# Kernel optimization log

Measured on AMD Instinct MI355X. Metric: run time of the kernel, lower is better.

Reference implementation:

```python
import jax, jax.numpy as jnp
import numpy as np

D_MODEL = 1024
N_HEADS = 16
N_EXPERTS = 8
TOP_K = 2
EXPERT_HIDDEN = D_MODEL * 4 // N_EXPERTS  # 512, per MoELayer default


def layer_norm(x, g, b, eps=1e-5):
    mu = jnp.mean(x, axis=-1, keepdims=True)
    var = jnp.var(x, axis=-1, keepdims=True)
    return (x - mu) * jax.lax.rsqrt(var + eps) * g + b


def setup_inputs() -> dict:
    key = jax.random.key(0)
    ks = jax.random.split(key, 12)
    s = 1.0 / np.sqrt(D_MODEL)
    return {
        "x": jax.random.normal(ks[0], (2, 2048, D_MODEL), dtype=jnp.float32),
        "Wq": jax.random.normal(ks[1], (D_MODEL, D_MODEL), dtype=jnp.float32) * s,
        "Wk": jax.random.normal(ks[2], (D_MODEL, D_MODEL), dtype=jnp.float32) * s,
        "Wv": jax.random.normal(ks[3], (D_MODEL, D_MODEL), dtype=jnp.float32) * s,
        "Wo": jax.random.normal(ks[4], (D_MODEL, D_MODEL), dtype=jnp.float32) * s,
        "g1": jnp.ones((D_MODEL,), jnp.float32),
        "b1": jnp.zeros((D_MODEL,), jnp.float32),
        "g2": jnp.ones((D_MODEL,), jnp.float32),
        "b2": jnp.zeros((D_MODEL,), jnp.float32),
        "Wg": jax.random.normal(ks[5], (D_MODEL, N_EXPERTS), dtype=jnp.float32) * s,
        "W1": jax.random.normal(ks[6], (N_EXPERTS, D_MODEL, EXPERT_HIDDEN), dtype=jnp.float32) * s,
        "W2": jax.random.normal(ks[7], (N_EXPERTS, EXPERT_HIDDEN, D_MODEL), dtype=jnp.float32) * (1.0 / np.sqrt(EXPERT_HIDDEN)),
    }


def reference(x, Wq, Wk, Wv, Wo, g1, b1, g2, b2, Wg, W1, W2):
    B, S, D = x.shape
    H, dk = N_HEADS, D // N_HEADS

    # ---- pre-norm attention + residual (dropout = identity in eval) ----
    xn = layer_norm(x, g1, b1)
    q = (xn @ Wq).reshape(B, S, H, dk).transpose(0, 2, 1, 3)  # [B,H,S,dk]
    k = (xn @ Wk).reshape(B, S, H, dk).transpose(0, 2, 1, 3)
    v = (xn @ Wv).reshape(B, S, H, dk).transpose(0, 2, 1, 3)
    scores = jnp.einsum("bhqd,bhkd->bhqk", q, k) / np.sqrt(dk)
    attn = jax.nn.softmax(scores, axis=-1)
    o = jnp.einsum("bhqk,bhkd->bhqd", attn, v)
    o = o.transpose(0, 2, 1, 3).reshape(B, S, D) @ Wo
    x = x + o

    # ---- pre-norm MoE + residual ----
    xn2 = layer_norm(x, g2, b2)
    xf = xn2.reshape(B * S, D)  # [T, D]
    gate = xf @ Wg  # [T, E]
    topv, topi = jax.lax.top_k(gate, TOP_K)  # [T, K]
    probs = jax.nn.softmax(topv, axis=-1)    # softmax over top-k scores
    # dense combine weights [T, E] (top-k indices are distinct)
    cw = jnp.sum(jax.nn.one_hot(topi, N_EXPERTS, dtype=xf.dtype) * probs[..., None], axis=1)
    h = jax.nn.relu(jnp.einsum("td,edh->teh", xf, W1))  # [T,E,Hid]
    y = jnp.einsum("teh,ehd->ted", h, W2)               # [T,E,D]
    moe = jnp.einsum("ted,te->td", y, cw).reshape(B, S, D)
    return x + moe
```

## Files before the change

### kernel.cpp

```cpp
#include <hip/hip_runtime.h>

typedef __attribute__((ext_vector_type(8))) _Float16 f16x8;
typedef __attribute__((ext_vector_type(4))) _Float16 f16x4;
typedef __attribute__((ext_vector_type(2))) _Float16 f16x2;
typedef __attribute__((ext_vector_type(2))) __fp16 fp16x2_n;
typedef __attribute__((ext_vector_type(8))) short bf16x8;
typedef __attribute__((ext_vector_type(4))) float f32x4;
typedef __attribute__((ext_vector_type(4))) unsigned short u16x4;
typedef __attribute__((ext_vector_type(4))) float fx4;

#define D_MODEL 1024
#define N_HEADS 16
#define SEQ 2048
#define TOKENS 4096
#define N_EXP 8
#define EHID 512
#define LO_S 2048.0f
#define INV_LO (1.0f / 2048.0f)
#define QSCALE 0.18033688011112043f
#define DTHR 11.0f

__device__ inline unsigned short f2bf(float f) {
  union { float f; unsigned u; } v; v.f = f;
  unsigned u = v.u;
  return (unsigned short)((u + 0x7FFFu + ((u >> 16) & 1u)) >> 16);
}

__device__ inline float bf2f(unsigned short b) {
  union { unsigned u; float f; } v; v.u = ((unsigned)b) << 16;
  return v.f;
}

__device__ inline void split16(float v, _Float16& h, _Float16& l) {
  h = (_Float16)v;
  l = (_Float16)((v - (float)h) * LO_S);
}

__device__ inline void split2(float a, float b, f16x2& h, f16x2& l) {
  fp16x2_n hn = __builtin_amdgcn_cvt_pkrtz(a, b);
  h = __builtin_bit_cast(f16x2, hn);
  fp16x2_n ln = __builtin_amdgcn_cvt_pkrtz((a - (float)h[0]) * LO_S, (b - (float)h[1]) * LO_S);
  l = __builtin_bit_cast(f16x2, ln);
}

__device__ inline void gload_lds16(const void* g, void* lds) {
  __builtin_amdgcn_global_load_lds((const __attribute__((address_space(1))) void*)g,
                                   (__attribute__((address_space(3))) void*)lds, 16, 0, 0);
}

__global__ __launch_bounds__(256) void prep_ln_kernel(const float* __restrict__ x, const float* __restrict__ g1,
                                                      const float* __restrict__ b1,
                                                      _Float16* __restrict__ xh, _Float16* __restrict__ xl,
                                                      const float* __restrict__ Wq, const float* __restrict__ Wk,
                                                      const float* __restrict__ Wv, const float* __restrict__ Wo,
                                                      const float* __restrict__ W1, const float* __restrict__ W2,
                                                      _Float16* __restrict__ qkvh, _Float16* __restrict__ qkvl,
                                                      _Float16* __restrict__ woh, _Float16* __restrict__ wol,
                                                      unsigned short* __restrict__ W1T, unsigned short* __restrict__ W2T,
                                                      int* __restrict__ cnt, int* __restrict__ perm) {
  int bb = blockIdx.x;
  if (bb < 4096) {
    int t = bb, tid = threadIdx.x;
    const float* row = x + (size_t)t * D_MODEL;
    fx4 v = *(const fx4*)(row + tid * 4);
    float s = v[0] + v[1] + v[2] + v[3];
    float s2 = v[0]*v[0] + v[1]*v[1] + v[2]*v[2] + v[3]*v[3];
    #pragma unroll
    for (int off = 1; off < 64; off <<= 1) { s += __shfl_xor(s, off); s2 += __shfl_xor(s2, off); }
    __shared__ float red[8];
    int wv = tid >> 6, wl = tid & 63;
    if (wl == 0) { red[wv] = s; red[4 + wv] = s2; }
    __syncthreads();
    s = red[0] + red[1] + red[2] + red[3];
    s2 = red[4] + red[5] + red[6] + red[7];
    float mu = s * (1.f / 1024.f);
    float var = s2 * (1.f / 1024.f) - mu * mu;
    float rstd = rsqrtf(var + 1e-5f);
    int kk = tid * 4;
    f16x4 oh, ol;
    #pragma unroll
    for (int c = 0; c < 4; c++) {
      float y = (v[c] - mu) * rstd * g1[kk + c] + b1[kk + c];
      _Float16 h, lo; split16(y, h, lo);
      oh[c] = h; ol[c] = lo;
    }
    *(f16x4*)(xh + (size_t)t * D_MODEL + kk) = oh;
    *(f16x4*)(xl + (size_t)t * D_MODEL + kk) = ol;
    return;
  }
  int b = bb - 4096;
  if (b >= 12288) {
    int i = (b - 12288) * 256 + threadIdx.x;
    if (i < 8) cnt[i] = 0;
    if (i < 8704) perm[i] = 0;
    return;
  }
  __shared__ float tile[32][33];
  int tx = threadIdx.x & 31, ty = threadIdx.x >> 5;
  if (b < 4096) {
    int z = b >> 10, rem = b & 1023;
    int c0 = (rem & 31) * 32, r0 = (rem >> 5) * 32;
    const float* src = (z == 0) ? Wq : (z == 1) ? Wk : (z == 2) ? Wv : Wo;
    _Float16* dh = (z < 3) ? qkvh + (size_t)z * 1048576 : woh;
    _Float16* dl = (z < 3) ? qkvl + (size_t)z * 1048576 : wol;
    #pragma unroll
    for (int i = 0; i < 4; i++) tile[ty + 8*i][tx] = src[(size_t)(r0 + ty + 8*i) * 1024 + c0 + tx];
    __syncthreads();
    #pragma unroll
    for (int i = 0; i < 4; i++) {
      float v = tile[tx][ty + 8*i];
      _Float16 h, lo; split16(v, h, lo);
      size_t idx = (size_t)(c0 + ty + 8*i) * 1024 + r0 + tx;
      dh[idx] = h; dl[idx] = lo;
    }
  } else if (b < 8192) {
    int q = b - 4096, z = q >> 9, rem = q & 511;
    int c0 = (rem & 15) * 32, r0 = (rem >> 4) * 32;
    const float* src = W1 + (size_t)z * 524288;
    unsigned short* dst = W1T + (size_t)z * 524288;
    #pragma unroll
    for (int i = 0; i < 4; i++) tile[ty + 8*i][tx] = src[(size_t)(r0 + ty + 8*i) * 512 + c0 + tx];
    __syncthreads();
    #pragma unroll
    for (int i = 0; i < 4; i++) dst[(size_t)(c0 + ty + 8*i) * 1024 + r0 + tx] = f2bf(tile[tx][ty + 8*i]);
  } else {
    int q = b - 8192, z = q >> 9, rem = q & 511;
    int c0 = (rem & 31) * 32, r0 = (rem >> 5) * 32;
    const float* src = W2 + (size_t)z * 524288;
    unsigned short* dst = W2T + (size_t)z * 524288;
    #pragma unroll
    for (int i = 0; i < 4; i++) tile[ty + 8*i][tx] = src[(size_t)(r0 + ty + 8*i) * 1024 + c0 + tx];
    __syncthreads();
    #pragma unroll
    for (int i = 0; i < 4; i++) dst[(size_t)(c0 + ty + 8*i) * 512 + r0 + tx] = f2bf(tile[tx][ty + 8*i]);
  }
}

__device__ inline void gemm128s(const _Float16* __restrict__ Ah, const _Float16* __restrict__ Al,
                                const _Float16* __restrict__ Bh, const _Float16* __restrict__ Bl,
                                int lda, int ldb, int K, int bm, int bn,
                                _Float16* lsbuf, f32x4 (&acc)[4][4], f32x4 (&accx)[4][4]) {
  const int tid = threadIdx.x, w = tid >> 6, l = tid & 63, lr = l & 15, lg = l >> 4;
  const int wr = (w >> 1) * 64, wc = (w & 1) * 64;
  int ca = (((tid & 3) ^ ((tid >> 3) & 3)) * 8);
  int ra0 = tid >> 2, ra1 = 64 + (tid >> 2);
  const _Float16* gA0 = Ah + (size_t)(bm + ra0) * lda + ca;
  const _Float16* gA1 = Ah + (size_t)(bm + ra1) * lda + ca;
  const _Float16* gA2 = Al + (size_t)(bm + ra0) * lda + ca;
  const _Float16* gA3 = Al + (size_t)(bm + ra1) * lda + ca;
  const _Float16* gB0 = Bh + (size_t)(bn + ra0) * ldb + ca;
  const _Float16* gB1 = Bh + (size_t)(bn + ra1) * ldb + ca;
  const _Float16* gB2 = Bl + (size_t)(bn + ra0) * ldb + ca;
  const _Float16* gB3 = Bl + (size_t)(bn + ra1) * ldb + ca;
  char* base = (char*)lsbuf;
  const int wo = w * 1024;
#define STAGE8(bb_, ko) do { \
    gload_lds16(gA0 + (ko), (bb_) + wo);         gload_lds16(gA1 + (ko), (bb_) + 4096 + wo);  \
    gload_lds16(gA2 + (ko), (bb_) + 8192 + wo);  gload_lds16(gA3 + (ko), (bb_) + 12288 + wo); \
    gload_lds16(gB0 + (ko), (bb_) + 16384 + wo); gload_lds16(gB1 + (ko), (bb_) + 20480 + wo); \
    gload_lds16(gB2 + (ko), (bb_) + 24576 + wo); gload_lds16(gB3 + (ko), (bb_) + 28672 + wo); } while (0)
  STAGE8(base, 0);
  __syncthreads();
  const int swzB = ((lg ^ ((lr >> 1) & 3)) << 4);
  int cur = 0;
  for (int ko = 0; ko < K; ko += 32) {
    char* bR = base + cur * 32768;
    if (ko + 32 < K) STAGE8(base + (cur ^ 1) * 32768, ko + 32);
    f16x8 ah[4], al4[4], bh4[4], bl4[4];
    #pragma unroll
    for (int m = 0; m < 4; m++) {
      int roff = (wr + m * 16 + lr) * 64 + swzB;
      ah[m]  = *(const f16x8*)(bR + roff);
      al4[m] = *(const f16x8*)(bR + 8192 + roff);
    }
    #pragma unroll
    for (int n = 0; n < 4; n++) {
      int roff = (wc + n * 16 + lr) * 64 + swzB;
      bh4[n] = *(const f16x8*)(bR + 16384 + roff);
      bl4[n] = *(const f16x8*)(bR + 24576 + roff);
    }
    __builtin_amdgcn_s_setprio(1);
    #pragma unroll
    for (int m = 0; m < 4; m++)
      #pragma unroll
      for (int n = 0; n < 4; n++) {
        acc[m][n]  = __builtin_amdgcn_mfma_f32_16x16x32_f16(ah[m], bh4[n], acc[m][n], 0, 0, 0);
        accx[m][n] = __builtin_amdgcn_mfma_f32_16x16x32_f16(ah[m], bl4[n], accx[m][n], 0, 0, 0);
        accx[m][n] = __builtin_amdgcn_mfma_f32_16x16x32_f16(al4[m], bh4[n], accx[m][n], 0, 0, 0);
      }
    __builtin_amdgcn_s_setprio(0);
    __syncthreads();
    cur ^= 1;
  }
#undef STAGE8
}

__global__ __launch_bounds__(256) void gemm_qkv_kernel(const _Float16* __restrict__ xh, const _Float16* __restrict__ xl,
                                                       const _Float16* __restrict__ Wh, const _Float16* __restrict__ Wl,
                                                       _Float16* __restrict__ qh, _Float16* __restrict__ ql,
                                                       _Float16* __restrict__ kh, _Float16* __restrict__ kl,
                                                       _Float16* __restrict__ vh, _Float16* __restrict__ vl) {
  __shared__ _Float16 ls[32768];
  f32x4 acc[4][4] = {}, accx[4][4] = {};
  int bid = blockIdx.x;
  int sw = (bid & 7) * 96 + (bid >> 3);
  int bm = (sw & 31) * 128, bn = (sw >> 5) * 128;
  gemm128s(xh, xl, Wh, Wl, 1024, 1024, 1024, bm, bn, ls, acc, accx);
  const int tid = threadIdx.x, w = tid >> 6, l = tid & 63, lr = l & 15, lg = l >> 4;
  const int wr = (w >> 1) * 64, wc = (w & 1) * 64;
  #pragma unroll
  for (int m = 0; m < 4; m++) {
    int row0 = bm + wr + m * 16 + lg * 4;
    #pragma unroll
    for (int n = 0; n < 4; n++) {
      int col = bn + wc + n * 16 + lr;
      int mat = col >> 10;
      int c = col & 1023, h = c >> 6, d = c & 63;
      if (mat == 2) {
        int bb = row0 >> 11, ss = row0 & 2047;
        int tile = ss >> 5, kvs = ss & 31;
        f16x4 ph, pl;
        #pragma unroll
        for (int j = 0; j < 4; j++) {
          float v = acc[m][n][j] + accx[m][n][j] * INV_LO;
          _Float16 hh, ll; split16(v, hh, ll);
          ph[j] = hh; pl[j] = ll;
        }
        size_t base = ((size_t)(bb * N_HEADS + h) * 64 + tile) * 2048;
        int off = d * 32 + ((((kvs >> 3) ^ ((d >> 1) & 3)) << 3) | (kvs & 7));
        *(f16x4*)(vh + base + off) = ph;
        *(f16x4*)(vl + base + off) = pl;
      } else if (mat == 1) {
        #pragma unroll
        for (int j = 0; j < 4; j++) {
          float v = acc[m][n][j] + accx[m][n][j] * INV_LO;
          _Float16 hh, ll; split16(v, hh, ll);
          int t = row0 + j, bb = t >> 11, ss = t & 2047;
          int tile = ss >> 5, r = ss & 31;
          size_t base = ((size_t)(bb * N_HEADS + h) * 64 + tile) * 2048;
          int off = r * 64 + ((((d >> 3) ^ (r & 7)) << 3) | (d & 7));
          kh[base + off] = hh; kl[base + off] = ll;
        }
      } else {
        #pragma unroll
        for (int j = 0; j < 4; j++) {
          float v = (acc[m][n][j] + accx[m][n][j] * INV_LO) * QSCALE;
          _Float16 hh, ll; split16(v, hh, ll);
          int t = row0 + j, bb = t >> 11, ss = t & 2047;
          size_t idx = ((size_t)(bb * N_HEADS + h) * SEQ + ss) * 64 + d;
          qh[idx] = hh; ql[idx] = ll;
        }
      }
    }
  }
}

__global__ __launch_bounds__(256, 4) void flash_kernel(const _Float16* __restrict__ qhp, const _Float16* __restrict__ qlp,
                                                       const _Float16* __restrict__ khs, const _Float16* __restrict__ kls,
                                                       const _Float16* __restrict__ vhs, const _Float16* __restrict__ vls,
                                                       _Float16* __restrict__ oh, _Float16* __restrict__ ol) {
  __shared__ _Float16 lsKV[2][8192];
  __shared__ _Float16 lsP[4][2][512];
  int wgid = blockIdx.x;
  int xcd = wgid & 7, kk = wgid >> 3;
  int bh = xcd * 4 + (kk >> 5), qt = kk & 31;
  int tid = threadIdx.x, w = tid >> 6, l = tid & 63, lr = l & 15, lg = l >> 4;
  int q0 = qt * 64 + w * 16;
  const _Float16* qhb = qhp + (size_t)bh * SEQ * 64;
  const _Float16* qlb = qlp + (size_t)bh * SEQ * 64;
  f16x8 qfh[2], qfl[2];
  #pragma unroll
  for (int ks = 0; ks < 2; ks++) {
    size_t idx = (size_t)(q0 + lr) * 64 + ks * 32 + lg * 8;
    qfh[ks] = *(const f16x8*)(qhb + idx);
    qfl[ks] = *(const f16x8*)(qlb + idx);
  }
  const _Float16* splane = (w == 0) ? khs : (w == 1) ? kls : (w == 2) ? vhs : vls;
  const _Float16* sbase = splane + (size_t)bh * 131072 + l * 8;

  f32x4 acc[4] = {}, accx[4] = {};
  float mst = -1e30f, lstp = 0.f;

  {
    const _Float16* sp = sbase;
    _Float16* dd = &lsKV[0][w * 2048];
    gload_lds16(sp, dd); gload_lds16(sp + 512, dd + 512);
    gload_lds16(sp + 1024, dd + 1024); gload_lds16(sp + 1536, dd + 1536);
  }
  __syncthreads();

  for (int t = 0; t < 64; t++) {
    int bR = t & 1;
    if (t < 63) {
      const _Float16* sp = sbase + (size_t)(t + 1) * 2048;
      _Float16* dd = &lsKV[bR ^ 1][w * 2048];
      gload_lds16(sp, dd); gload_lds16(sp + 512, dd + 512);
      gload_lds16(sp + 1024, dd + 1024); gload_lds16(sp + 1536, dd + 1536);
    }
    char* bufB = (char*)&lsKV[bR][0];

    f32x4 s[2] = {}, sx[2] = {};
    #pragma unroll
    for (int ks = 0; ks < 2; ks++) {
      f16x8 kfh[2], kfl[2];
      #pragma unroll
      for (int m = 0; m < 2; m++) {
        int off = (m * 16 + lr) * 128 + (((ks * 4 + lg) ^ (lr & 7)) << 4);
        kfh[m] = *(const f16x8*)(bufB + off);
        kfl[m] = *(const f16x8*)(bufB + 4096 + off);
      }
      __builtin_amdgcn_s_setprio(1);
      #pragma unroll
      for (int m = 0; m < 2; m++) {
        s[m]  = __builtin_amdgcn_mfma_f32_16x16x32_f16(kfh[m], qfh[ks], s[m], 0, 0, 0);
        sx[m] = __builtin_amdgcn_mfma_f32_16x16x32_f16(kfh[m], qfl[ks], sx[m], 0, 0, 0);
        sx[m] = __builtin_amdgcn_mfma_f32_16x16x32_f16(kfl[m], qfh[ks], sx[m], 0, 0, 0);
      }
      __builtin_amdgcn_s_setprio(0);
    }

    float tm = -3e38f;
    #pragma unroll
    for (int m = 0; m < 2; m++)
      #pragma unroll
      for (int j = 0; j < 4; j++) {
        s[m][j] += sx[m][j] * INV_LO;
        tm = fmaxf(tm, s[m][j]);
      }
    if (!__all(tm - mst <= DTHR)) {
      tm = fmaxf(tm, __shfl_xor(tm, 16));
      tm = fmaxf(tm, __shfl_xor(tm, 32));
      float mnew = fmaxf(mst, tm);
      float corr = exp2f(mst - mnew);
      #pragma unroll
      for (int m2 = 0; m2 < 4; m2++)
        #pragma unroll
        for (int j = 0; j < 4; j++) { acc[m2][j] *= corr; accx[m2][j] *= corr; }
      lstp *= corr;
      mst = mnew;
    }
    #pragma unroll
    for (int m = 0; m < 2; m++) {
      #pragma unroll
      for (int j = 0; j < 4; j++) {
        float p = exp2f(s[m][j] - mst);
        lstp += p;
        s[m][j] = p;
      }
      f16x2 h01, h23, l01, l23;
      split2(s[m][0], s[m][1], h01, l01);
      split2(s[m][2], s[m][3], h23, l23);
      f16x4 ph, pl;
      ph[0] = h01[0]; ph[1] = h01[1]; ph[2] = h23[0]; ph[3] = h23[1];
      pl[0] = l01[0]; pl[1] = l01[1]; pl[2] = l23[0]; pl[3] = l23[1];
      int boff = lr * 64 + ((((m * 2 + (lg >> 1)) ^ ((lr >> 1) & 3)) << 4) | ((lg & 1) * 8));
      *(f16x4*)((char*)&lsP[w][0][0] + boff) = ph;
      *(f16x4*)((char*)&lsP[w][1][0] + boff) = pl;
    }

    int poff = lr * 64 + ((lg ^ ((lr >> 1) & 3)) << 4);
    f16x8 pfh = *(const f16x8*)((char*)&lsP[w][0][0] + poff);
    f16x8 pfl = *(const f16x8*)((char*)&lsP[w][1][0] + poff);
    __builtin_amdgcn_s_setprio(1);
    #pragma unroll
    for (int m2 = 0; m2 < 4; m2++) {
      int voff = (m2 * 16 + lr) * 64 + ((lg ^ ((lr >> 1) & 3)) << 4);
      f16x8 vfh = *(const f16x8*)(bufB + 8192 + voff);
      f16x8 vfl = *(const f16x8*)(bufB + 12288 + voff);
      acc[m2]  = __builtin_amdgcn_mfma_f32_16x16x32_f16(vfh, pfh, acc[m2], 0, 0, 0);
      accx[m2] = __builtin_amdgcn_mfma_f32_16x16x32_f16(vfh, pfl, accx[m2], 0, 0, 0);
      accx[m2] = __builtin_amdgcn_mfma_f32_16x16x32_f16(vfl, pfh, accx[m2], 0, 0, 0);
    }
    __builtin_amdgcn_s_setprio(0);
    __syncthreads();
  }

  float lst = lstp + __shfl_xor(lstp, 16);
  lst += __shfl_xor(lst, 32);
  float inv = 1.f / lst;
  int b = bh >> 4, h = bh & 15;
  int tkn = b * SEQ + q0 + lr;
  #pragma unroll
  for (int m2 = 0; m2 < 4; m2++) {
    f16x4 ph, pl;
    #pragma unroll
    for (int j = 0; j < 4; j++) {
      float o = (acc[m2][j] + accx[m2][j] * INV_LO) * inv;
      _Float16 hh, ll; split16(o, hh, ll);
      ph[j] = hh; pl[j] = ll;
    }
    size_t idx = (size_t)tkn * D_MODEL + h * 64 + m2 * 16 + lg * 4;
    *(f16x4*)(oh + idx) = ph;
    *(f16x4*)(ol + idx) = pl;
  }
}

__global__ __launch_bounds__(256) void gemm_oproj_kernel(const _Float16* __restrict__ ah, const _Float16* __restrict__ al,
                                                         const _Float16* __restrict__ Wh, const _Float16* __restrict__ Wl,
                                                         const float* __restrict__ x, float* __restrict__ out) {
  __shared__ _Float16 ls[32768];
  f32x4 acc[4][4] = {}, accx[4][4] = {};
  int bid = blockIdx.x;
  int sw = (bid & 7) * 32 + (bid >> 3);
  int bm = (sw & 31) * 128, bn = (sw >> 5) * 128;
  gemm128s(ah, al, Wh, Wl, 1024, 1024, 1024, bm, bn, ls, acc, accx);
  const int tid = threadIdx.x, w = tid >> 6, l = tid & 63, lr = l & 15, lg = l >> 4;
  const int wr = (w >> 1) * 64, wc = (w & 1) * 64;
  #pragma unroll
  for (int m = 0; m < 4; m++) {
    int row0 = bm + wr + m * 16 + lg * 4;
    #pragma unroll
    for (int n = 0; n < 4; n++) {
      int col = bn + wc + n * 16 + lr;
      #pragma unroll
      for (int j = 0; j < 4; j++) {
        size_t idx = (size_t)(row0 + j) * D_MODEL + col;
        out[idx] = (acc[m][n][j] + accx[m][n][j] * INV_LO) + x[idx];
      }
    }
  }
}

__global__ __launch_bounds__(256) void gate_kernel(const float* __restrict__ x1, const float* __restrict__ Wg,
                                                   const float* __restrict__ g2, const float* __restrict__ b2,
                                                   unsigned short* __restrict__ xn2,
                                                   int* __restrict__ cnt, int* __restrict__ topi,
                                                   float* __restrict__ topw) {
  int t = blockIdx.x * 4 + (threadIdx.x >> 6);
  int l = threadIdx.x & 63;
  const float* row = x1 + (size_t)t * D_MODEL;
  fx4 v[4];
  float s = 0.f, s2 = 0.f;
  #pragma unroll
  for (int i = 0; i < 4; i++) {
    v[i] = *(const fx4*)(row + l * 16 + i * 4);
    #pragma unroll
    for (int c = 0; c < 4; c++) { s += v[i][c]; s2 += v[i][c] * v[i][c]; }
  }
  #pragma unroll
  for (int off = 1; off < 64; off <<= 1) { s += __shfl_xor(s, off); s2 += __shfl_xor(s2, off); }
  float mu = s * (1.f / 1024.f);
  float var = s2 * (1.f / 1024.f) - mu * mu;
  float rstd = rsqrtf(var + 1e-5f);
  float a8[8] = {0,0,0,0,0,0,0,0};
  #pragma unroll
  for (int i = 0; i < 4; i++) {
    u16x4 ox;
    #pragma unroll
    for (int c = 0; c < 4; c++) {
      int kk = l * 16 + i * 4 + c;
      float xv = (v[i][c] - mu) * rstd * g2[kk] + b2[kk];
      ox[c] = f2bf(xv);
      const float* wr_ = Wg + (size_t)kk * 8;
      fx4 wa = *(const fx4*)wr_;
      fx4 wb = *(const fx4*)(wr_ + 4);
      a8[0] += xv * wa[0]; a8[1] += xv * wa[1]; a8[2] += xv * wa[2]; a8[3] += xv * wa[3];
      a8[4] += xv * wb[0]; a8[5] += xv * wb[1]; a8[6] += xv * wb[2]; a8[7] += xv * wb[3];
    }
    *(u16x4*)(xn2 + (size_t)t * D_MODEL + l * 16 + i * 4) = ox;
  }
  #pragma unroll
  for (int e = 0; e < 8; e++)
    #pragma unroll
    for (int off = 1; off < 64; off <<= 1) a8[e] += __shfl_xor(a8[e], off);
  if (l == 0) {
    int i0 = 0; float v0 = a8[0];
    #pragma unroll
    for (int e = 1; e < 8; e++) if (a8[e] > v0) { v0 = a8[e]; i0 = e; }
    int i1 = -1; float v1 = -3.4e38f;
    #pragma unroll
    for (int e = 0; e < 8; e++) if (e != i0 && a8[e] > v1) { v1 = a8[e]; i1 = e; }
    float p0 = 1.f / (1.f + __expf(v1 - v0));
    topi[t * 2] = i0; topi[t * 2 + 1] = i1;
    topw[t * 2] = p0; topw[t * 2 + 1] = 1.f - p0;
    atomicAdd(&cnt[i0], 1); atomicAdd(&cnt[i1], 1);
  }
}

__global__ __launch_bounds__(256) void scatter_kernel(const int* __restrict__ topi, const int* __restrict__ cnt,
                                                      int* __restrict__ perm, int* __restrict__ slot_of) {
  int e = blockIdx.x, tid = threadIdx.x;
  __shared__ int basesh;
  __shared__ int wsum[4];
  if (tid == 0) {
    int a = 0;
    for (int i = 0; i < e; i++) a += ((cnt[i] + 63) >> 6) << 6;
    basesh = a;
  }
  __syncthreads();
  for (int seg = 0; seg < 8192; seg += 256) {
    int a = seg + tid;
    int match = (topi[a] == e) ? 1 : 0;
    unsigned long long bal = __ballot(match);
    int wl = tid & 63, wv = tid >> 6;
    int lanepre = __popcll(bal & ((1ULL << wl) - 1ULL));
    if (wl == 0) wsum[wv] = __popcll(bal);
    __syncthreads();
    int wpre = 0;
    for (int i = 0; i < wv; i++) wpre += wsum[i];
    int total = wsum[0] + wsum[1] + wsum[2] + wsum[3];
    if (match) {
      int pos = basesh + wpre + lanepre;
      perm[pos] = a >> 1;
      slot_of[a] = pos;
    }
    __syncthreads();
    if (tid == 0) basesh += total;
    __syncthreads();
  }
}

__global__ __launch_bounds__(512) void moe_ffn_kernel(const unsigned short* __restrict__ xn2,
                                                      const unsigned short* __restrict__ W1T,
                                                      const unsigned short* __restrict__ W2T,
                                                      const int* __restrict__ cnt,
                                                      const int* __restrict__ perm,
                                                      unsigned short* __restrict__ y) {
  int bid = blockIdx.x;
  int e = -1, lt = bid, off = 0;
  for (int i = 0; i < 8; i++) {
    int nt = (cnt[i] + 63) >> 6;
    if (lt < nt) { e = i; break; }
    lt -= nt; off += nt << 6;
  }
  if (e < 0) return;
  int slot0 = off + lt * 64;

  __shared__ int t_sh[64];
  __shared__ unsigned short lsX[64 * 128];
  __shared__ unsigned short hsh[64 * 264];
  int tid = threadIdx.x, w = tid >> 6, l = tid & 63, lr = l & 15, lg = l >> 4;
  if (tid < 64) t_sh[tid] = perm[slot0 + tid];
  __syncthreads();

  const unsigned short* W1e = W1T + (size_t)e * EHID * D_MODEL;
  const unsigned short* W2e = W2T + (size_t)e * D_MODEL * EHID;

  f32x4 acc2[4][8] = {};
  for (int h = 0; h < 2; h++) {
    f32x4 acc1[4][2] = {};
    for (int kc = 0; kc < 8; kc++) {
      __syncthreads();
      #pragma unroll
      for (int L = 0; L < 2; L++) {
        int u = tid + 512 * L;
        int r = u >> 4, sp = u & 15;
        int cs = (sp & 8) | ((sp & 7) ^ (r & 7));
        gload_lds16(xn2 + (size_t)t_sh[r] * D_MODEL + kc * 128 + cs * 8, (char*)lsX + u * 16);
      }
      __syncthreads();
      #pragma unroll
      for (int kst = 0; kst < 4; kst++) {
        bf16x8 a[4];
        #pragma unroll
        for (int m = 0; m < 4; m++) {
          int row = m * 16 + lr;
          int slot = kst * 4 + lg;
          int cs = (slot & 8) | ((slot & 7) ^ (row & 7));
          a[m] = *(const bf16x8*)((char*)lsX + row * 256 + cs * 16);
        }
        int ko = kc * 128 + kst * 32;
        #pragma unroll
        for (int n = 0; n < 2; n++) {
          bf16x8 bb = *(const bf16x8*)(W1e + (size_t)(h * 256 + w * 32 + n * 16 + lr) * D_MODEL + ko + lg * 8);
          #pragma unroll
          for (int m = 0; m < 4; m++)
            acc1[m][n] = __builtin_amdgcn_mfma_f32_16x16x32_bf16(a[m], bb, acc1[m][n], 0, 0, 0);
        }
      }
    }
    __syncthreads();
    #pragma unroll
    for (int m = 0; m < 4; m++)
      #pragma unroll
      for (int n = 0; n < 2; n++)
        #pragma unroll
        for (int j = 0; j < 4; j++)
          hsh[(m*16 + lg*4 + j) * 264 + w * 32 + n * 16 + lr] = f2bf(fmaxf(acc1[m][n][j], 0.f));
    __syncthreads();
    for (int k2 = 0; k2 < 256; k2 += 32) {
      bf16x8 a2[4];
      #pragma unroll
      for (int m = 0; m < 4; m++) a2[m] = *(const bf16x8*)(hsh + (m*16 + lr) * 264 + k2 + lg * 8);
      #pragma unroll
      for (int n = 0; n < 8; n++) {
        bf16x8 bb = *(const bf16x8*)(W2e + (size_t)(w * 128 + n * 16 + lr) * EHID + h * 256 + k2 + lg * 8);
        #pragma unroll
        for (int m = 0; m < 4; m++)
          acc2[m][n] = __builtin_amdgcn_mfma_f32_16x16x32_bf16(a2[m], bb, acc2[m][n], 0, 0, 0);
      }
    }
  }
  #pragma unroll
  for (int m = 0; m < 4; m++)
    #pragma unroll
    for (int j = 0; j < 4; j++) {
      int r = m * 16 + lg * 4 + j;
      #pragma unroll
      for (int n = 0; n < 8; n++)
        y[(size_t)(slot0 + r) * D_MODEL + w * 128 + n * 16 + lr] = f2bf(acc2[m][n][j]);
    }
}

__global__ __launch_bounds__(256) void combine_kernel(const unsigned short* __restrict__ y, const int* __restrict__ slot_of,
                                                      const float* __restrict__ topw, float* __restrict__ out) {
  int t = blockIdx.x * 4 + (threadIdx.x >> 6);
  int l = threadIdx.x & 63;
  int s0 = slot_of[t * 2], s1 = slot_of[t * 2 + 1];
  float w0 = topw[t * 2], w1 = topw[t * 2 + 1];
  const unsigned short* y0 = y + (size_t)s0 * D_MODEL + l * 16;
  const unsigned short* y1 = y + (size_t)s1 * D_MODEL + l * 16;
  float* o = out + (size_t)t * D_MODEL + l * 16;
  #pragma unroll
  for (int i = 0; i < 4; i++) {
    u16x4 av = *(const u16x4*)(y0 + i * 4);
    u16x4 bv = *(const u16x4*)(y1 + i * 4);
    fx4 d = *(const fx4*)(o + i * 4);
    #pragma unroll
    for (int j = 0; j < 4; j++) d[j] += w0 * bf2f(av[j]) + w1 * bf2f(bv[j]);
    *(fx4*)(o + i * 4) = d;
  }
}

#define MB (1u << 20)
extern "C" void kernel_launch(void* const* d_in, const int* in_sizes, int n_in,
                              void* d_out, int out_size, void* d_ws, size_t ws_size,
                              hipStream_t stream) {
  const float* x  = (const float*)d_in[0];
  const float* Wq = (const float*)d_in[1];
  const float* Wk = (const float*)d_in[2];
  const float* Wv = (const float*)d_in[3];
  const float* Wo = (const float*)d_in[4];
  const float* g1 = (const float*)d_in[5];
  const float* b1 = (const float*)d_in[6];
  const float* g2 = (const float*)d_in[7];
  const float* b2 = (const float*)d_in[8];
  const float* Wg = (const float*)d_in[9];
  const float* W1 = (const float*)d_in[10];
  const float* W2 = (const float*)d_in[11];
  float* out = (float*)d_out;

  char* ws = (char*)d_ws;
  _Float16* xn1h = (_Float16*)(ws + 0*MB);
  _Float16* xn1l = (_Float16*)(ws + 8*MB);
  _Float16* Wqkh = (_Float16*)(ws + 16*MB);
  _Float16* Wqkl = (_Float16*)(ws + 22*MB);
  _Float16* Woh  = (_Float16*)(ws + 28*MB);
  _Float16* Wol  = (_Float16*)(ws + 30*MB);
  _Float16* qhb  = (_Float16*)(ws + 32*MB);
  _Float16* qlb  = (_Float16*)(ws + 40*MB);
  _Float16* khb  = (_Float16*)(ws + 48*MB);
  _Float16* klb  = (_Float16*)(ws + 56*MB);
  _Float16* vhb  = (_Float16*)(ws + 64*MB);
  _Float16* vlb  = (_Float16*)(ws + 72*MB);
  unsigned short* xn2 = (unsigned short*)(ws + 80*MB);
  unsigned short* W1T = (unsigned short*)(ws + 88*MB);
  unsigned short* W2T = (unsigned short*)(ws + 96*MB);
  char* misc = ws + 104*MB;
  int*   topi    = (int*)(misc);
  float* topw    = (float*)(misc + 32768);
  int*   slot_of = (int*)(misc + 65536);
  int*   cnt     = (int*)(misc + 98304);
  int*   perm    = (int*)(misc + 98368);
  unsigned short* ybuf = (unsigned short*)(ws + 32*MB);
  _Float16* attnh = xn1h;
  _Float16* attnl = xn1l;

  prep_ln_kernel<<<16419, 256, 0, stream>>>(x, g1, b1, xn1h, xn1l,
                                            Wq, Wk, Wv, Wo, W1, W2,
                                            Wqkh, Wqkl, Woh, Wol, W1T, W2T, cnt, perm);

  gemm_qkv_kernel<<<768, 256, 0, stream>>>(xn1h, xn1l, Wqkh, Wqkl, qhb, qlb, khb, klb, vhb, vlb);
  flash_kernel<<<1024, 256, 0, stream>>>(qhb, qlb, khb, klb, vhb, vlb, attnh, attnl);
  gemm_oproj_kernel<<<256, 256, 0, stream>>>(attnh, attnl, Woh, Wol, x, out);

  gate_kernel<<<1024, 256, 0, stream>>>(out, Wg, g2, b2, xn2, cnt, topi, topw);
  scatter_kernel<<<8, 256, 0, stream>>>(topi, cnt, perm, slot_of);
  moe_ffn_kernel<<<136, 512, 0, stream>>>(xn2, W1T, W2T, cnt, perm, ybuf);
  combine_kernel<<<1024, 256, 0, stream>>>(ybuf, slot_of, topw, out);

  (void)in_sizes; (void)n_in; (void)out_size; (void)ws_size;
}
```

Measured before the change: 526.5 us.

## Process two query tiles per flash block and parallelize MoE scatter by segment

The flash attention kernel now handles 128 query rows per workgroup (two 64-row sub-tiles) instead of 64. Each K/V tile loaded into LDS is therefore reused twice, which halves global K/V traffic and the grid size. The MoE scatter is split into 64 blocks (expert × segment) using per-segment counts gathered in the gate kernel, replacing 8 serial blocks. The costs are higher register pressure in flash, fewer workgroups to fill the GPU, and extra atomics in the gate kernel.

Result: slower. 647.4 us (+23.0%).

```diff
diff --git a/kernel.cpp b/kernel.cpp
--- a/kernel.cpp
+++ b/kernel.cpp
@@ -57,7 +57,8 @@
                                                       _Float16* __restrict__ qkvh, _Float16* __restrict__ qkvl,
                                                       _Float16* __restrict__ woh, _Float16* __restrict__ wol,
                                                       unsigned short* __restrict__ W1T, unsigned short* __restrict__ W2T,
-                                                      int* __restrict__ cnt, int* __restrict__ perm) {
+                                                      int* __restrict__ cnt, int* __restrict__ cnt8,
+                                                      int* __restrict__ perm) {
   int bb = blockIdx.x;
   if (bb < 4096) {
     int t = bb, tid = threadIdx.x;
@@ -92,6 +93,7 @@
   if (b >= 12288) {
     int i = (b - 12288) * 256 + threadIdx.x;
     if (i < 8) cnt[i] = 0;
+    if (i < 64) cnt8[i] = 0;
     if (i < 8704) perm[i] = 0;
     return;
   }
@@ -263,23 +265,25 @@
   __shared__ _Float16 lsP[4][2][512];
   int wgid = blockIdx.x;
   int xcd = wgid & 7, kk = wgid >> 3;
-  int bh = xcd * 4 + (kk >> 5), qt = kk & 31;
+  int bh = xcd * 4 + (kk >> 4), qt = kk & 15;
   int tid = threadIdx.x, w = tid >> 6, l = tid & 63, lr = l & 15, lg = l >> 4;
-  int q0 = qt * 64 + w * 16;
+  int q0 = qt * 128 + w * 16;
   const _Float16* qhb = qhp + (size_t)bh * SEQ * 64;
   const _Float16* qlb = qlp + (size_t)bh * SEQ * 64;
-  f16x8 qfh[2], qfl[2];
-  #pragma unroll
-  for (int ks = 0; ks < 2; ks++) {
-    size_t idx = (size_t)(q0 + lr) * 64 + ks * 32 + lg * 8;
-    qfh[ks] = *(const f16x8*)(qhb + idx);
-    qfl[ks] = *(const f16x8*)(qlb + idx);
-  }
+  f16x8 qfh[2][2], qfl[2][2];
+  #pragma unroll
+  for (int tq = 0; tq < 2; tq++)
+    #pragma unroll
+    for (int ks = 0; ks < 2; ks++) {
+      size_t idx = (size_t)(q0 + tq * 64 + lr) * 64 + ks * 32 + lg * 8;
+      qfh[tq][ks] = *(const f16x8*)(qhb + idx);
+      qfl[tq][ks] = *(const f16x8*)(qlb + idx);
+    }
   const _Float16* splane = (w == 0) ? khs : (w == 1) ? kls : (w == 2) ? vhs : vls;
   const _Float16* sbase = splane + (size_t)bh * 131072 + l * 8;
 
-  f32x4 acc[4] = {}, accx[4] = {};
-  float mst = -1e30f, lstp = 0.f;
+  f32x4 acc[2][4] = {}, accx[2][4] = {};
+  float mst[2] = {-1e30f, -1e30f}, lstp[2] = {0.f, 0.f};
 
   {
     const _Float16* sp = sbase;
@@ -299,99 +303,105 @@
     }
     char* bufB = (char*)&lsKV[bR][0];
 
-    f32x4 s[2] = {}, sx[2] = {};
-    #pragma unroll
-    for (int ks = 0; ks < 2; ks++) {
-      f16x8 kfh[2], kfl[2];
+    #pragma unroll
+    for (int tq = 0; tq < 2; tq++) {
+      f32x4 s[2] = {}, sx[2] = {};
+      #pragma unroll
+      for (int ks = 0; ks < 2; ks++) {
+        f16x8 kfh[2], kfl[2];
+        #pragma unroll
+        for (int m = 0; m < 2; m++) {
+          int off = (m * 16 + lr) * 128 + (((ks * 4 + lg) ^ (lr & 7)) << 4);
+          kfh[m] = *(const f16x8*)(bufB + off);
+          kfl[m] = *(const f16x8*)(bufB + 4096 + off);
+        }
+        __builtin_amdgcn_s_setprio(1);
+        #pragma unroll
+        for (int m = 0; m < 2; m++) {
+          s[m]  = __builtin_amdgcn_mfma_f32_16x16x32_f16(kfh[m], qfh[tq][ks], s[m], 0, 0, 0);
+          sx[m] = __builtin_amdgcn_mfma_f32_16x16x32_f16(kfh[m], qfl[tq][ks], sx[m], 0, 0, 0);
+          sx[m] = __builtin_amdgcn_mfma_f32_16x16x32_f16(kfl[m], qfh[tq][ks], sx[m], 0, 0, 0);
+        }
+        __builtin_amdgcn_s_setprio(0);
+      }
+
+      float tm = -3e38f;
+      #pragma unroll
+      for (int m = 0; m < 2; m++)
+        #pragma unroll
+        for (int j = 0; j < 4; j++) {
+          s[m][j] += sx[m][j] * INV_LO;
+          tm = fmaxf(tm, s[m][j]);
+        }
+      if (!__all(tm - mst[tq] <= DTHR)) {
+        tm = fmaxf(tm, __shfl_xor(tm, 16));
+        tm = fmaxf(tm, __shfl_xor(tm, 32));
+        float mnew = fmaxf(mst[tq], tm);
+        float corr = exp2f(mst[tq] - mnew);
+        #pragma unroll
+        for (int m2 = 0; m2 < 4; m2++)
+          #pragma unroll
+          for (int j = 0; j < 4; j++) { acc[tq][m2][j] *= corr; accx[tq][m2][j] *= corr; }
+        lstp[tq] *= corr;
+        mst[tq] = mnew;
+      }
       #pragma unroll
       for (int m = 0; m < 2; m++) {
-        int off = (m * 16 + lr) * 128 + (((ks * 4 + lg) ^ (lr & 7)) << 4);
-        kfh[m] = *(const f16x8*)(bufB + off);
-        kfl[m] = *(const f16x8*)(bufB + 4096 + off);
-      }
+        #pragma unroll
+        for (int j = 0; j < 4; j++) {
+          float p = exp2f(s[m][j] - mst[tq]);
+          lstp[tq] += p;
+          s[m][j] = p;
+        }
+        f16x2 h01, h23, l01, l23;
+        split2(s[m][0], s[m][1], h01, l01);
+        split2(s[m][2], s[m][3], h23, l23);
+        f16x4 ph, pl;
+        ph[0] = h01[0]; ph[1] = h01[1]; ph[2] = h23[0]; ph[3] = h23[1];
+        pl[0] = l01[0]; pl[1] = l01[1]; pl[2] = l23[0]; pl[3] = l23[1];
+        int boff = lr * 64 + ((((m * 2 + (lg >> 1)) ^ ((lr >> 1) & 3)) << 4) | ((lg & 1) * 8));
+        *(f16x4*)((char*)&lsP[w][0][0] + boff) = ph;
+        *(f16x4*)((char*)&lsP[w][1][0] + boff) = pl;
+      }
+
+      int poff = lr * 64 + ((lg ^ ((lr >> 1) & 3)) << 4);
+      f16x8 pfh = *(const f16x8*)((char*)&lsP[w][0][0] + poff);
+      f16x8 pfl = *(const f16x8*)((char*)&lsP[w][1][0] + poff);
       __builtin_amdgcn_s_setprio(1);
       #pragma unroll
-      for (int m = 0; m < 2; m++) {
-        s[m]  = __builtin_amdgcn_mfma_f32_16x16x32_f16(kfh[m], qfh[ks], s[m], 0, 0, 0);
-        sx[m] = __builtin_amdgcn_mfma_f32_16x16x32_f16(kfh[m], qfl[ks], sx[m], 0, 0, 0);
-        sx[m] = __builtin_amdgcn_mfma_f32_16x16x32_f16(kfl[m], qfh[ks], sx[m], 0, 0, 0);
+      for (int m2 = 0; m2 < 4; m2++) {
+        int voff = (m2 * 16 + lr) * 64 + ((lg ^ ((lr >> 1) & 3)) << 4);
+        f16x8 vfh = *(const f16x8*)(bufB + 8192 + voff);
+        f16x8 vfl = *(const f16x8*)(bufB + 12288 + voff);
+        acc[tq][m2]  = __builtin_amdgcn_mfma_f32_16x16x32_f16(vfh, pfh, acc[tq][m2], 0, 0, 0);
+        accx[tq][m2] = __builtin_amdgcn_mfma_f32_16x16x32_f16(vfh, pfl, accx[tq][m2], 0, 0, 0);
+        accx[tq][m2] = __builtin_amdgcn_mfma_f32_16x16x32_f16(vfl, pfh, accx[tq][m2], 0, 0, 0);
       }
       __builtin_amdgcn_s_setprio(0);
     }
-
-    float tm = -3e38f;
-    #pragma unroll
-    for (int m = 0; m < 2; m++)
+    __syncthreads();
+  }
+
+  int b = bh >> 4, h = bh & 15;
+  #pragma unroll
+  for (int tq = 0; tq < 2; tq++) {
+    float lst = lstp[tq] + __shfl_xor(lstp[tq], 16);
+    lst += __shfl_xor(lst, 32);
+    float inv = 1.f / lst;
+    int tkn = b * SEQ + q0 + tq * 64 + lr;
+    #pragma unroll
+    for (int m2 = 0; m2 < 4; m2++) {
+      f16x4 ph, pl;
       #pragma unroll
       for (int j = 0; j < 4; j++) {
-        s[m][j] += sx[m][j] * INV_LO;
-        tm = fmaxf(tm, s[m][j]);
-      }
-    if (!__all(tm - mst <= DTHR)) {
-      tm = fmaxf(tm, __shfl_xor(tm, 16));
-      tm = fmaxf(tm, __shfl_xor(tm, 32));
-      float mnew = fmaxf(mst, tm);
-      float corr = exp2f(mst - mnew);
-      #pragma unroll
-      for (int m2 = 0; m2 < 4; m2++)
-        #pragma unroll
-        for (int j = 0; j < 4; j++) { acc[m2][j] *= corr; accx[m2][j] *= corr; }
-      lstp *= corr;
-      mst = mnew;
-    }
-    #pragma unroll
-    for (int m = 0; m < 2; m++) {
-      #pragma unroll
-      for (int j = 0; j < 4; j++) {
-        float p = exp2f(s[m][j] - mst);
-        lstp += p;
-        s[m][j] = p;
-      }
-      f16x2 h01, h23, l01, l23;
-      split2(s[m][0], s[m][1], h01, l01);
-      split2(s[m][2], s[m][3], h23, l23);
-      f16x4 ph, pl;
-      ph[0] = h01[0]; ph[1] = h01[1]; ph[2] = h23[0]; ph[3] = h23[1];
-      pl[0] = l01[0]; pl[1] = l01[1]; pl[2] = l23[0]; pl[3] = l23[1];
-      int boff = lr * 64 + ((((m * 2 + (lg >> 1)) ^ ((lr >> 1) & 3)) << 4) | ((lg & 1) * 8));
-      *(f16x4*)((char*)&lsP[w][0][0] + boff) = ph;
-      *(f16x4*)((char*)&lsP[w][1][0] + boff) = pl;
-    }
-
-    int poff = lr * 64 + ((lg ^ ((lr >> 1) & 3)) << 4);
-    f16x8 pfh = *(const f16x8*)((char*)&lsP[w][0][0] + poff);
-    f16x8 pfl = *(const f16x8*)((char*)&lsP[w][1][0] + poff);
-    __builtin_amdgcn_s_setprio(1);
-    #pragma unroll
-    for (int m2 = 0; m2 < 4; m2++) {
-      int voff = (m2 * 16 + lr) * 64 + ((lg ^ ((lr >> 1) & 3)) << 4);
-      f16x8 vfh = *(const f16x8*)(bufB + 8192 + voff);
-      f16x8 vfl = *(const f16x8*)(bufB + 12288 + voff);
-      acc[m2]  = __builtin_amdgcn_mfma_f32_16x16x32_f16(vfh, pfh, acc[m2], 0, 0, 0);
-      accx[m2] = __builtin_amdgcn_mfma_f32_16x16x32_f16(vfh, pfl, accx[m2], 0, 0, 0);
-      accx[m2] = __builtin_amdgcn_mfma_f32_16x16x32_f16(vfl, pfh, accx[m2], 0, 0, 0);
-    }
-    __builtin_amdgcn_s_setprio(0);
-    __syncthreads();
-  }
-
-  float lst = lstp + __shfl_xor(lstp, 16);
-  lst += __shfl_xor(lst, 32);
-  float inv = 1.f / lst;
-  int b = bh >> 4, h = bh & 15;
-  int tkn = b * SEQ + q0 + lr;
-  #pragma unroll
-  for (int m2 = 0; m2 < 4; m2++) {
-    f16x4 ph, pl;
-    #pragma unroll
-    for (int j = 0; j < 4; j++) {
-      float o = (acc[m2][j] + accx[m2][j] * INV_LO) * inv;
-      _Float16 hh, ll; split16(o, hh, ll);
-      ph[j] = hh; pl[j] = ll;
-    }
-    size_t idx = (size_t)tkn * D_MODEL + h * 64 + m2 * 16 + lg * 4;
-    *(f16x4*)(oh + idx) = ph;
-    *(f16x4*)(ol + idx) = pl;
+        float o = (acc[tq][m2][j] + accx[tq][m2][j] * INV_LO) * inv;
+        _Float16 hh, ll; split16(o, hh, ll);
+        ph[j] = hh; pl[j] = ll;
+      }
+      size_t idx = (size_t)tkn * D_MODEL + h * 64 + m2 * 16 + lg * 4;
+      *(f16x4*)(oh + idx) = ph;
+      *(f16x4*)(ol + idx) = pl;
+    }
   }
 }
 
@@ -424,8 +434,8 @@
 __global__ __launch_bounds__(256) void gate_kernel(const float* __restrict__ x1, const float* __restrict__ Wg,
                                                    const float* __restrict__ g2, const float* __restrict__ b2,
                                                    unsigned short* __restrict__ xn2,
-                                                   int* __restrict__ cnt, int* __restrict__ topi,
-                                                   float* __restrict__ topw) {
+                                                   int* __restrict__ cnt, int* __restrict__ cnt8,
+                                                   int* __restrict__ topi, float* __restrict__ topw) {
   int t = blockIdx.x * 4 + (threadIdx.x >> 6);
   int l = threadIdx.x & 63;
   const float* row = x1 + (size_t)t * D_MODEL;
@@ -473,23 +483,29 @@
     float p0 = 1.f / (1.f + __expf(v1 - v0));
     topi[t * 2] = i0; topi[t * 2 + 1] = i1;
     topw[t * 2] = p0; topw[t * 2 + 1] = 1.f - p0;
+    int seg = t >> 9;
     atomicAdd(&cnt[i0], 1); atomicAdd(&cnt[i1], 1);
+    atomicAdd(&cnt8[i0 * 8 + seg], 1); atomicAdd(&cnt8[i1 * 8 + seg], 1);
   }
 }
 
 __global__ __launch_bounds__(256) void scatter_kernel(const int* __restrict__ topi, const int* __restrict__ cnt,
+                                                      const int* __restrict__ cnt8,
                                                       int* __restrict__ perm, int* __restrict__ slot_of) {
-  int e = blockIdx.x, tid = threadIdx.x;
+  int e = blockIdx.x & 7, seg = blockIdx.x >> 3;
+  int tid = threadIdx.x;
   __shared__ int basesh;
   __shared__ int wsum[4];
   if (tid == 0) {
     int a = 0;
     for (int i = 0; i < e; i++) a += ((cnt[i] + 63) >> 6) << 6;
+    for (int s = 0; s < seg; s++) a += cnt8[e * 8 + s];
     basesh = a;
   }
   __syncthreads();
-  for (int seg = 0; seg < 8192; seg += 256) {
-    int a = seg + tid;
+  int a0 = seg * 1024;
+  for (int segi = 0; segi < 1024; segi += 256) {
+    int a = a0 + segi + tid;
     int match = (topi[a] == e) ? 1 : 0;
     unsigned long long bal = __ballot(match);
     int wl = tid & 63, wv = tid >> 6;
@@ -661,21 +677,22 @@
   float* topw    = (float*)(misc + 32768);
   int*   slot_of = (int*)(misc + 65536);
   int*   cnt     = (int*)(misc + 98304);
-  int*   perm    = (int*)(misc + 98368);
+  int*   cnt8    = (int*)(misc + 98368);
+  int*   perm    = (int*)(misc + 98688);
   unsigned short* ybuf = (unsigned short*)(ws + 32*MB);
   _Float16* attnh = xn1h;
   _Float16* attnl = xn1l;
 
   prep_ln_kernel<<<16419, 256, 0, stream>>>(x, g1, b1, xn1h, xn1l,
                                             Wq, Wk, Wv, Wo, W1, W2,
-                                            Wqkh, Wqkl, Woh, Wol, W1T, W2T, cnt, perm);
+                                            Wqkh, Wqkl, Woh, Wol, W1T, W2T, cnt, cnt8, perm);
 
   gemm_qkv_kernel<<<768, 256, 0, stream>>>(xn1h, xn1l, Wqkh, Wqkl, qhb, qlb, khb, klb, vhb, vlb);
-  flash_kernel<<<1024, 256, 0, stream>>>(qhb, qlb, khb, klb, vhb, vlb, attnh, attnl);
+  flash_kernel<<<512, 256, 0, stream>>>(qhb, qlb, khb, klb, vhb, vlb, attnh, attnl);
   gemm_oproj_kernel<<<256, 256, 0, stream>>>(attnh, attnl, Woh, Wol, x, out);
 
-  gate_kernel<<<1024, 256, 0, stream>>>(out, Wg, g2, b2, xn2, cnt, topi, topw);
-  scatter_kernel<<<8, 256, 0, stream>>>(topi, cnt, perm, slot_of);
+  gate_kernel<<<1024, 256, 0, stream>>>(out, Wg, g2, b2, xn2, cnt, cnt8, topi, topw);
+  scatter_kernel<<<64, 256, 0, stream>>>(topi, cnt, cnt8, perm, slot_of);
   moe_ffn_kernel<<<136, 512, 0, stream>>>(xn2, W1T, W2T, cnt, perm, ybuf);
   combine_kernel<<<1024, 256, 0, stream>>>(ybuf, slot_of, topw, out);
 
```
